# Performance work log

Hardware: AMD Instinct MI355X
Metric: run time of the kernel (lower is better)

The kernel has to match this reference:

```python
import jax, jax.numpy as jnp
import numpy as np

P = 8          # patch_size
DIM = 256      # embed dim
HEADS = 8
HEAD_DIM = DIM // HEADS
CH = 3
PATCH_DIM = CH * P * P  # 192
INNER = int(4.0 * DIM)  # 1024
SCALE = HEAD_DIM ** -0.5


def sine_pos_embedding(n, c, dtype=jnp.float32):
    # standard 1D sinusoidal position encoding, shape (n, c)
    pos = jnp.arange(n, dtype=jnp.float32)[:, None]            # (n,1)
    div = jnp.exp(jnp.arange(0, c, 2, dtype=jnp.float32) * (-np.log(10000.0) / c))
    pe = jnp.zeros((n, c), dtype=jnp.float32)
    pe = pe.at[:, 0::2].set(jnp.sin(pos * div))
    pe = pe.at[:, 1::2].set(jnp.cos(pos * div))
    return pe.astype(dtype)


def patchify(x):
    # (B,C,H,W) -> (B, n, p1*p2*C), matching 'b c (h p1) (w p2) -> b (h w) (p1 p2 c)'
    B, C, H, W = x.shape
    hp, wp = H // P, W // P
    x = x.reshape(B, C, hp, P, wp, P)
    x = x.transpose(0, 2, 4, 3, 5, 1)        # (B, hp, wp, p1, p2, C)
    return x.reshape(B, hp * wp, P * P * C)


def unpatchify(x, hp, wp):
    # (B, n, p1*p2*C) -> (B, C, H, W)
    B = x.shape[0]
    x = x.reshape(B, hp, wp, P, P, CH)
    x = x.transpose(0, 5, 1, 3, 2, 4)        # (B, C, hp, p1, wp, p2)
    return x.reshape(B, CH, hp * P, wp * P)


def setup_inputs() -> dict:
    key = jax.random.key(0)
    ks = jax.random.split(key, 16)
    B, H, W = 8, 256, 256
    s = 0.02
    img0 = jax.random.normal(ks[0], (B, CH, H, W), dtype=jnp.float32)
    img1 = jax.random.normal(ks[1], (B, CH, H, W), dtype=jnp.float32)
    mask = jax.random.randint(ks[2], (B, 1, H, W), 0, 2).astype(jnp.float32)
    return {
        "img0": img0,
        "img1": img1,
        "mask": mask,
        "w_patch": jax.random.normal(ks[3], (PATCH_DIM, DIM), jnp.float32) * s,
        "b_patch": jnp.zeros((DIM,), jnp.float32),
        "w_kv": jax.random.normal(ks[4], (DIM, 2 * DIM), jnp.float32) * s,
        "b_kv": jnp.zeros((2 * DIM,), jnp.float32),
        "w_qv": jax.random.normal(ks[5], (DIM, 2 * DIM), jnp.float32) * s,
        "b_qv": jnp.zeros((2 * DIM,), jnp.float32),
        "w_fc1": jax.random.normal(ks[6], (DIM, INNER), jnp.float32) * s,
        "b_fc1": jnp.zeros((INNER,), jnp.float32),
        "w_fc2": jax.random.normal(ks[7], (INNER, PATCH_DIM), jnp.float32) * s,
        "b_fc2": jnp.zeros((PATCH_DIM,), jnp.float32),
    }


def reference(img0, img1, mask, w_patch, b_patch, w_kv, b_kv, w_qv, b_qv,
              w_fc1, b_fc1, w_fc2, b_fc2):
    B, C, H, W = img0.shape
    hp, wp = H // P, W // P
    n = hp * wp

    x0 = patchify(img0) @ w_patch + b_patch   # (B, n, dim)
    x1 = patchify(img1) @ w_patch + b_patch
    pe = sine_pos_embedding(n, DIM)
    x0 = x0 + pe
    x1 = x1 + pe

    # img0 -> k, v
    kv = (x0 @ w_kv + b_kv).reshape(B, n, 2, HEADS, HEAD_DIM)
    kv = kv.transpose(2, 0, 3, 1, 4)          # (2, B, heads, n, hd)
    k, v = kv[0], kv[1]

    # img1 -> q (v1 unused in forward, matching torch code)
    qv = (x1 @ w_qv + b_qv).reshape(B, n, 2, DIM).transpose(2, 0, 1, 3)
    q = qv[0].reshape(B, n, HEADS, HEAD_DIM).transpose(0, 2, 1, 3)  # (B, heads, n, hd)

    dots = jnp.einsum('bhqd,bhkd->bhqk', q, k) * SCALE  # (B, heads, n, n)

    # mask: (B,1,H,W) -> per-patch sum -> binary -> additive bias over key dim
    msum = mask.reshape(B, 1, hp, P, wp, P).sum(axis=(3, 5)).reshape(B, 1, n)
    bias = jnp.where(msum > 0, 0.0, -100.0)[:, :, None, :]  # (B,1,1,n)

    attn = jax.nn.softmax(dots + bias, axis=-1)
    out = jnp.einsum('bhqk,bhkd->bhqd', attn, v)
    out = out.transpose(0, 2, 1, 3).reshape(B, n, DIM)

    # mlp2: Linear -> GELU(exact) -> Linear
    h = jax.nn.gelu(out @ w_fc1 + b_fc1, approximate=False)
    res = h @ w_fc2 + b_fc2                   # (B, n, patch_dim)

    return unpatchify(res, hp, wp)            # (B, C, H, W)
```

## Files before the change

kernel.cpp:

```cpp
#include <hip/hip_runtime.h>
#include <cstdint>
#include <cstddef>

typedef __bf16 bf16_t;
typedef uint32_t u32;
typedef __bf16 bf16x4 __attribute__((ext_vector_type(4)));
typedef __bf16 bf16x8 __attribute__((ext_vector_type(8)));
typedef float f32x4 __attribute__((ext_vector_type(4)));
typedef float f32x16 __attribute__((ext_vector_type(16)));

__device__ __forceinline__ void gload_lds16(const bf16_t* g, bf16_t* l) {
  __builtin_amdgcn_global_load_lds((const __attribute__((address_space(1))) void*)g,
                                   (__attribute__((address_space(3))) void*)l,
                                   16, 0, 0);
}

__device__ __forceinline__ f32x4 mfma16(bf16x8 a, bf16x8 b, f32x4 c) {
  return __builtin_amdgcn_mfma_f32_16x16x32_bf16(a, b, c, 0, 0, 0);
}
__device__ __forceinline__ f32x16 mfma32(bf16x8 a, bf16x8 b, f32x16 c) {
  return __builtin_amdgcn_mfma_f32_32x32x16_bf16(a, b, c, 0, 0, 0);
}

#define LOG2E 1.4426950408889634f

__global__ __launch_bounds__(256)
void prep_all(const float* __restrict__ img0, const float* __restrict__ img1,
              const float* __restrict__ mask,
              const float* __restrict__ wp, const float* __restrict__ wkv,
              const float* __restrict__ wqv, const float* __restrict__ wfc1,
              const float* __restrict__ wfc2,
              bf16_t* __restrict__ xp0, bf16_t* __restrict__ xp1,
              float* __restrict__ pe, float* __restrict__ bias,
              bf16_t* __restrict__ wpT, bf16_t* __restrict__ wkvT,
              bf16_t* __restrict__ wqT, bf16_t* __restrict__ wfc1T,
              bf16_t* __restrict__ wfc2T) {
  __shared__ float tl[64 * 65];
  int bid = blockIdx.x, tid = threadIdx.x;
  if (bid < 1536) {
    int imgsel = bid >= 768;
    int t = (bid - (imgsel ? 768 : 0)) * 256 + tid;
    const float* img = imgsel ? img1 : img0;
    bf16_t* xp = imgsel ? xp1 : xp0;
    int wpp = t & 31, p1 = (t >> 5) & 7, hp = (t >> 8) & 31, rest = t >> 13;
    int b = rest / 3, c = rest - b * 3;
    const float* src = img + (((size_t)(b * 3 + c) * 256 + hp * 8 + p1) * 256 + wpp * 8);
    float4 v0 = *(const float4*)src;
    float4 v1 = *(const float4*)(src + 4);
    int row = b * 1024 + hp * 32 + wpp;
    bf16_t* dst = xp + (size_t)row * 192 + p1 * 24 + c;
    dst[0]  = (bf16_t)v0.x; dst[3]  = (bf16_t)v0.y; dst[6]  = (bf16_t)v0.z; dst[9]  = (bf16_t)v0.w;
    dst[12] = (bf16_t)v1.x; dst[15] = (bf16_t)v1.y; dst[18] = (bf16_t)v1.z; dst[21] = (bf16_t)v1.w;
  } else if (bid < 2560) {
    int t = bid - 1536, c = tid;
    int i2 = c & ~1;
    float div = expf((float)i2 * (-9.210340371976184f / 256.0f));
    float arg = (float)t * div;
    pe[t * 256 + c] = (c & 1) ? cosf(arg) : sinf(arg);
  } else if (bid < 2592) {
    int g = (bid - 2560) * 256 + tid;
    int b = g >> 10, t = g & 1023, hp = t >> 5, wpp = t & 31;
    const float* mp = mask + ((size_t)b * 256 + hp * 8) * 256 + wpp * 8;
    float s = 0.f;
    #pragma unroll
    for (int p1 = 0; p1 < 8; p1++) {
      float4 a = *(const float4*)(mp + p1 * 256);
      float4 c = *(const float4*)(mp + p1 * 256 + 4);
      s += a.x + a.y + a.z + a.w + c.x + c.y + c.z + c.w;
    }
    bias[g] = (s > 0.f) ? 0.f : (-100.f * LOG2E);
  } else {
    int i = bid - 2592;
    const float* src; bf16_t* dst; int srcN, dstK, NT;
    if (i >= 172) {
      int j = i - 172;
      bf16_t* p = wfc2T + 192 * 1024 + j * 8192 + tid * 32;
      bf16x8 z;
      #pragma unroll
      for (int e = 0; e < 8; e++) z[e] = (bf16_t)0.0f;
      *(bf16x8*)(p) = z; *(bf16x8*)(p + 8) = z;
      *(bf16x8*)(p + 16) = z; *(bf16x8*)(p + 24) = z;
      return;
    }
    if (i < 12)       { src = wp;   dst = wpT;   srcN = 256;  dstK = 192;  NT = 4; }
    else if (i < 44)  { i -= 12;  src = wkv;  dst = wkvT;  srcN = 512;  dstK = 256;  NT = 8; }
    else if (i < 60)  { i -= 44;  src = wqv;  dst = wqT;   srcN = 512;  dstK = 256;  NT = 4; }
    else if (i < 124) { i -= 60;  src = wfc1; dst = wfc1T; srcN = 1024; dstK = 256;  NT = 16; }
    else              { i -= 124; src = wfc2; dst = wfc2T; srcN = 192;  dstK = 1024; NT = 3; }
    int kt = i / NT, nt = i - kt * NT;
    #pragma unroll
    for (int j = 0; j < 4; j++) {
      int r = (tid >> 4) + 16 * j, c = (tid & 15) * 4;
      float4 v = *(const float4*)(src + (size_t)(kt * 64 + r) * srcN + nt * 64 + c);
      tl[r * 65 + c] = v.x; tl[r * 65 + c + 1] = v.y;
      tl[r * 65 + c + 2] = v.z; tl[r * 65 + c + 3] = v.w;
    }
    __syncthreads();
    #pragma unroll
    for (int j = 0; j < 16; j++) {
      int flat = tid + 256 * j;
      int n_l = flat >> 6, k_l = flat & 63;
      dst[(size_t)(nt * 64 + n_l) * dstK + kt * 64 + k_l] = (bf16_t)tl[k_l * 65 + n_l];
    }
  }
}

template<int EPI, int BN>
__global__ __launch_bounds__(256)
void gemm_bt(const bf16_t* __restrict__ A_, const bf16_t* __restrict__ A2,
             const bf16_t* __restrict__ Bt_, const bf16_t* __restrict__ Bt2,
             int M, int N, int K,
             const float* __restrict__ bias_, const float* __restrict__ bias2,
             const float* __restrict__ pe,
             bf16_t* __restrict__ out_b, bf16_t* __restrict__ out_b2,
             bf16_t* __restrict__ out_b3, float* __restrict__ out_f) {
  constexpr int NF = BN / 32;
  __shared__ bf16_t alds[4 * 64 * 8];
  __shared__ bf16_t blds[4 * BN * 8];
  const int tid = threadIdx.x;
  const int lane = tid & 63, wid = tid >> 6;
  const int ln15 = lane & 15, hi = lane >> 4;
  const int brow = blockIdx.x * 64;
  int bcol = blockIdx.y * BN;
  const bf16_t* A = A_;
  const bf16_t* Bt = Bt_;
  const float* bias = bias_;
  bool qpart = false;
  if (EPI == 0 && blockIdx.z) A = A2;
  if (EPI == 5 && blockIdx.y >= 4) {
    qpart = true; A = A2; Bt = Bt2; bias = bias2; bcol -= 512;
  }
  const int wr = wid >> 1, wc = wid & 1;

  f32x4 acc[2][NF];
  #pragma unroll
  for (int m = 0; m < 2; m++)
    #pragma unroll
    for (int n = 0; n < NF; n++) acc[m][n] = (f32x4){0.f, 0.f, 0.f, 0.f};

  for (int k0 = 0; k0 < K; k0 += 32) {
    {
      int c = tid; int row = c & 63; int kb = c >> 6;
      const bf16_t* g = A + (size_t)(brow + row) * K + k0 + kb * 8;
      gload_lds16(g, &alds[(wid * 64) * 8]);
    }
    #pragma unroll
    for (int s = 0; s < BN / 64; s++) {
      int c = tid + s * 256; int row = c & (BN - 1); int kb = c / BN;
      const bf16_t* g = Bt + (size_t)(bcol + row) * K + k0 + kb * 8;
      gload_lds16(g, &blds[(wid * 64 + s * 256) * 8]);
    }
    __syncthreads();
    bf16x8 af[2], bfr[NF];
    #pragma unroll
    for (int m = 0; m < 2; m++)
      af[m] = *(const bf16x8*)&alds[(hi * 64 + wr * 32 + m * 16 + ln15) * 8];
    #pragma unroll
    for (int n = 0; n < NF; n++)
      bfr[n] = *(const bf16x8*)&blds[(hi * BN + wc * (BN / 2) + n * 16 + ln15) * 8];
    #pragma unroll
    for (int m = 0; m < 2; m++)
      #pragma unroll
      for (int n = 0; n < NF; n++)
        acc[m][n] = mfma16(af[m], bfr[n], acc[m][n]);
    __syncthreads();
  }

  #pragma unroll
  for (int m = 0; m < 2; m++) {
    #pragma unroll
    for (int n = 0; n < NF; n++) {
      #pragma unroll
      for (int r = 0; r < 4; r++) {
        int grow = brow + wr * 32 + m * 16 + hi * 4 + r;
        int gcol = bcol + wc * (BN / 2) + n * 16 + ln15;
        float v = acc[m][n][r];
        if (EPI == 0) {
          v += bias[gcol] + pe[(grow & 1023) * 256 + gcol];
          bf16_t* outx = blockIdx.z ? out_b2 : out_b;
          outx[(size_t)grow * N + gcol] = (bf16_t)v;
        } else if (EPI == 5) {
          v += bias[gcol];
          int b = grow >> 10, t = grow & 1023;
          if (!qpart) {
            if (gcol < 256) {
              int h = gcol >> 5, d = gcol & 31;
              out_b[(((size_t)(b * 8 + h) * 1024 + t) << 5) + d] = (bf16_t)v;
            } else {
              int c2 = gcol - 256; int h = c2 >> 5, d = c2 & 31;
              out_b2[(((size_t)(b * 8 + h) * 32 + d) << 10) + t] = (bf16_t)v;
            }
          } else {
            v *= (0.17677669529663687f * LOG2E);
            int h = gcol >> 5, d = gcol & 31;
            out_b3[(((size_t)(b * 8 + h) * 1024 + t) << 5) + d] = (bf16_t)v;
          }
        } else if (EPI == 3) {
          v += bias[gcol];
          float gg = 0.5f * v * (1.0f + erff(v * 0.7071067811865476f));
          out_b[(size_t)grow * N + gcol] = (bf16_t)gg;
        } else if (EPI == 4) {
          if (gcol < 192) {
            v += bias[gcol];
            int b = grow >> 10, t = grow & 1023;
            int hp = t >> 5, wpp = t & 31;
            int p = gcol / 3; int c = gcol - p * 3;
            int p1 = p >> 3, p2 = p & 7;
            out_f[(((size_t)(b * 3 + c) * 256 + hp * 8 + p1) * 256) + wpp * 8 + p2] = v;
          }
        }
      }
    }
  }
}

union PW { u32 w[4]; bf16x8 v; };

__device__ __forceinline__ u32 pkbf(float a, float b) {
  union { bf16_t h[2]; u32 w; } u;
  u.h[0] = (bf16_t)a; u.h[1] = (bf16_t)b;
  return u.w;
}

__device__ __forceinline__ void pl32swap(u32& a, u32& b) {
  asm volatile("v_permlane32_swap_b32 %0, %1" : "+v"(a), "+v"(b));
}

__global__ __launch_bounds__(256, 4)
void attn_kernel(const bf16_t* __restrict__ q, const bf16_t* __restrict__ k,
                 const bf16_t* __restrict__ vt, const float* __restrict__ bias,
                 bf16_t* __restrict__ out) {
  __shared__ float OL[4][32][34];
  __shared__ float LS[4][64];
  int tid = threadIdx.x, lane = tid & 63, wid = tid >> 6;
  int l31 = lane & 31, g = lane >> 5;
  int x = blockIdx.x & 7;
  int bh = (((blockIdx.x >> 3) & 7) << 3) | x;
  int qt = blockIdx.x >> 6;
  int b = bh >> 3, h = bh & 7;
  int q0 = qt * 32;
  const bf16_t* qp = q + ((size_t)bh * 1024 + q0 + l31) * 32;
  bf16x8 qf0 = *(const bf16x8*)(qp + g * 8);
  bf16x8 qf1 = *(const bf16x8*)(qp + 16 + g * 8);
  const bf16_t* kbase = k + (size_t)bh * 32768;
  const bf16_t* vbase = vt + (size_t)bh * 32768;
  const float* bb = bias + b * 1024;

  f32x16 acc;
  #pragma unroll
  for (int r = 0; r < 16; r++) acc[r] = 0.f;
  float lsum = 0.f;

  #pragma unroll
  for (int kt = 0; kt < 8; kt++) {
    int k0 = (wid * 8 + kt) * 32;
    bf16x8 kA = *(const bf16x8*)(kbase + (size_t)(k0 + l31) * 32 + g * 8);
    bf16x8 kB = *(const bf16x8*)(kbase + (size_t)(k0 + l31) * 32 + 16 + g * 8);
    bf16x8 vA = *(const bf16x8*)(vbase + (size_t)l31 * 1024 + k0 + g * 8);
    bf16x8 vB = *(const bf16x8*)(vbase + (size_t)l31 * 1024 + k0 + 16 + g * 8);
    f32x4 c0 = *(const f32x4*)(bb + k0 + 4 * g);
    f32x4 c1 = *(const f32x4*)(bb + k0 + 8 + 4 * g);
    f32x4 c2 = *(const f32x4*)(bb + k0 + 16 + 4 * g);
    f32x4 c3 = *(const f32x4*)(bb + k0 + 24 + 4 * g);
    f32x16 S;
    S[0] = c0[0]; S[1] = c0[1]; S[2] = c0[2]; S[3] = c0[3];
    S[4] = c1[0]; S[5] = c1[1]; S[6] = c1[2]; S[7] = c1[3];
    S[8] = c2[0]; S[9] = c2[1]; S[10] = c2[2]; S[11] = c2[3];
    S[12] = c3[0]; S[13] = c3[1]; S[14] = c3[2]; S[15] = c3[3];
    S = mfma32(kA, qf0, S);
    S = mfma32(kB, qf1, S);
    float p[16];
    #pragma unroll
    for (int r = 0; r < 16; r++) p[r] = exp2f(S[r]);
    lsum += (((p[0] + p[1]) + (p[2] + p[3])) + ((p[4] + p[5]) + (p[6] + p[7]))) +
            (((p[8] + p[9]) + (p[10] + p[11])) + ((p[12] + p[13]) + (p[14] + p[15])));
    u32 w[8];
    #pragma unroll
    for (int j = 0; j < 8; j++) w[j] = pkbf(p[2 * j], p[2 * j + 1]);
    u32 xa = w[2], ya = w[0]; pl32swap(xa, ya);
    u32 xb = w[3], yb = w[1]; pl32swap(xb, yb);
    u32 xc = w[6], yc = w[4]; pl32swap(xc, yc);
    u32 xd = w[7], yd = w[5]; pl32swap(xd, yd);
    PW A0, A1;
    A0.w[0] = g ? xa : w[0];  A0.w[2] = g ? w[2] : ya;
    A0.w[1] = g ? xb : w[1];  A0.w[3] = g ? w[3] : yb;
    A1.w[0] = g ? xc : w[4];  A1.w[2] = g ? w[6] : yc;
    A1.w[1] = g ? xd : w[5];  A1.w[3] = g ? w[7] : yd;
    acc = mfma32(A0.v, vA, acc);
    acc = mfma32(A1.v, vB, acc);
  }

  #pragma unroll
  for (int r = 0; r < 16; r++) {
    int row = (r & 3) + 8 * (r >> 2) + 4 * g;
    OL[wid][row][l31] = acc[r];
  }
  LS[wid][lane] = lsum;
  __syncthreads();

  int qq = tid >> 3, d0 = (tid & 7) * 4;
  float l = 0.f;
  #pragma unroll
  for (int w2 = 0; w2 < 4; w2++) l += LS[w2][qq] + LS[w2][32 + qq];
  float o0 = 0.f, o1 = 0.f, o2 = 0.f, o3 = 0.f;
  #pragma unroll
  for (int w2 = 0; w2 < 4; w2++) {
    o0 += OL[w2][qq][d0];     o1 += OL[w2][qq][d0 + 1];
    o2 += OL[w2][qq][d0 + 2]; o3 += OL[w2][qq][d0 + 3];
  }
  float linv = 1.f / l;
  bf16x4 ov;
  ov[0] = (bf16_t)(o0 * linv); ov[1] = (bf16_t)(o1 * linv);
  ov[2] = (bf16_t)(o2 * linv); ov[3] = (bf16_t)(o3 * linv);
  *(bf16x4*)(out + ((size_t)b * 1024 + q0 + qq) * 256 + h * 32 + d0) = ov;
}

extern "C" void kernel_launch(void* const* d_in, const int* in_sizes, int n_in,
                              void* d_out, int out_size, void* d_ws, size_t ws_size,
                              hipStream_t stream) {
  (void)in_sizes; (void)n_in; (void)out_size; (void)ws_size;
  const float* img0    = (const float*)d_in[0];
  const float* img1    = (const float*)d_in[1];
  const float* mask    = (const float*)d_in[2];
  const float* w_patch = (const float*)d_in[3];
  const float* b_patch = (const float*)d_in[4];
  const float* w_kv    = (const float*)d_in[5];
  const float* b_kv    = (const float*)d_in[6];
  const float* w_qv    = (const float*)d_in[7];
  const float* b_qv    = (const float*)d_in[8];
  const float* w_fc1   = (const float*)d_in[9];
  const float* b_fc1   = (const float*)d_in[10];
  const float* w_fc2   = (const float*)d_in[11];
  const float* b_fc2   = (const float*)d_in[12];
  float* out = (float*)d_out;

  char* ws = (char*)d_ws;
  float*  pe    = (float*)(ws + 0);
  float*  bias  = (float*)(ws + 1048576);
  bf16_t* wpT   = (bf16_t*)(ws + 1081344);
  bf16_t* wkvT  = (bf16_t*)(ws + 1179648);
  bf16_t* wqT   = (bf16_t*)(ws + 1441792);
  bf16_t* wfc1T = (bf16_t*)(ws + 1572864);
  bf16_t* wfc2T = (bf16_t*)(ws + 2097152);
  bf16_t* xp0   = (bf16_t*)(ws + 2621440);
  bf16_t* xp1   = (bf16_t*)(ws + 5767168);
  bf16_t* x0    = (bf16_t*)(ws + 8912896);
  bf16_t* x1    = (bf16_t*)(ws + 13107200);
  bf16_t* kbuf  = (bf16_t*)(ws + 17301504);
  bf16_t* vtbuf = (bf16_t*)(ws + 21495808);
  bf16_t* qbuf  = (bf16_t*)(ws + 25690112);
  bf16_t* aout  = (bf16_t*)(ws + 29884416);
  bf16_t* hbuf  = (bf16_t*)(ws + 34078720);

  prep_all<<<2772, 256, 0, stream>>>(img0, img1, mask, w_patch, w_kv, w_qv, w_fc1, w_fc2,
                                     xp0, xp1, pe, bias, wpT, wkvT, wqT, wfc1T, wfc2T);

  gemm_bt<0, 64><<<dim3(128, 4, 2), 256, 0, stream>>>(xp0, xp1, wpT, nullptr, 8192, 256, 192,
                                                      b_patch, nullptr, pe, x0, x1, nullptr, nullptr);
  gemm_bt<5, 128><<<dim3(128, 6), 256, 0, stream>>>(x0, x1, wkvT, wqT, 8192, 512, 256,
                                                    b_kv, b_qv, nullptr, kbuf, vtbuf, qbuf, nullptr);

  attn_kernel<<<2048, 256, 0, stream>>>(qbuf, kbuf, vtbuf, bias, aout);

  gemm_bt<3, 128><<<dim3(128, 8), 256, 0, stream>>>(aout, nullptr, wfc1T, nullptr, 8192, 1024, 256,
                                                    b_fc1, nullptr, nullptr, hbuf, nullptr, nullptr, nullptr);
  gemm_bt<4, 64><<<dim3(128, 4), 256, 0, stream>>>(hbuf, nullptr, wfc2T, nullptr, 8192, 256, 1024,
                                                   b_fc2, nullptr, nullptr, nullptr, nullptr, nullptr, out);
}
```

Baseline: 122.9 us.

## Stage K/V tiles in LDS with double buffering and share them across query waves

The attention kernel is restructured. Before, each block of four waves split the 1024 keys for 32 queries and combined partial outputs through shared memory. Now each block covers 128 queries, one 32-query tile per wave, and every wave walks all keys. K and V^T chunks of 256 keys are staged into double-buffered, XOR-swizzled LDS with global_load_lds, so all four waves reuse the same K/V data. This removes the cross-wave output reduction and cuts global K/V traffic, but it uses more LDS, lowers occupancy to two blocks per CU, and launches four times fewer blocks.

```diff
diff --git a/kernel.cpp b/kernel.cpp
--- a/kernel.cpp
+++ b/kernel.cpp
@@ -226,19 +226,39 @@
   asm volatile("v_permlane32_swap_b32 %0, %1" : "+v"(a), "+v"(b));
 }
 
-__global__ __launch_bounds__(256, 4)
+__device__ __forceinline__ void stage_kv(const bf16_t* kbase, const bf16_t* vbase,
+                                         int ch, bf16_t* kl, bf16_t* vl,
+                                         int tid, int wid) {
+  #pragma unroll
+  for (int p = 0; p < 4; p++) {
+    int s = p * 256 + tid;
+    int row = s >> 2, cs = (s & 3) ^ (row & 3);
+    const bf16_t* src = kbase + (size_t)(ch * 256 + row) * 32 + cs * 8;
+    gload_lds16(src, kl + (size_t)(p * 256 + wid * 64) * 8);
+  }
+  #pragma unroll
+  for (int p = 0; p < 4; p++) {
+    int s = p * 256 + tid;
+    int row = s >> 5, cs = (s & 31) ^ row;
+    const bf16_t* src = vbase + (size_t)row * 1024 + ch * 256 + cs * 8;
+    gload_lds16(src, vl + (size_t)(p * 256 + wid * 64) * 8);
+  }
+}
+
+__global__ __launch_bounds__(256, 2)
 void attn_kernel(const bf16_t* __restrict__ q, const bf16_t* __restrict__ k,
                  const bf16_t* __restrict__ vt, const float* __restrict__ bias,
                  bf16_t* __restrict__ out) {
-  __shared__ float OL[4][32][34];
-  __shared__ float LS[4][64];
+  __shared__ bf16_t klds[2][1024 * 8];
+  __shared__ bf16_t vlds[2][1024 * 8];
+  __shared__ float LSL[4][32];
   int tid = threadIdx.x, lane = tid & 63, wid = tid >> 6;
   int l31 = lane & 31, g = lane >> 5;
-  int x = blockIdx.x & 7;
-  int bh = (((blockIdx.x >> 3) & 7) << 3) | x;
-  int qt = blockIdx.x >> 6;
+  int x = blockIdx.x & 7, idx = blockIdx.x >> 3;
+  int qt = idx & 7;
+  int bh = ((idx >> 3) << 3) | x;
   int b = bh >> 3, h = bh & 7;
-  int q0 = qt * 32;
+  int q0 = qt * 128 + wid * 32;
   const bf16_t* qp = q + ((size_t)bh * 1024 + q0 + l31) * 32;
   bf16x8 qf0 = *(const bf16x8*)(qp + g * 8);
   bf16x8 qf1 = *(const bf16x8*)(qp + 16 + g * 8);
@@ -251,68 +271,65 @@
   for (int r = 0; r < 16; r++) acc[r] = 0.f;
   float lsum = 0.f;
 
-  #pragma unroll
-  for (int kt = 0; kt < 8; kt++) {
-    int k0 = (wid * 8 + kt) * 32;
-    bf16x8 kA = *(const bf16x8*)(kbase + (size_t)(k0 + l31) * 32 + g * 8);
-    bf16x8 kB = *(const bf16x8*)(kbase + (size_t)(k0 + l31) * 32 + 16 + g * 8);
-    bf16x8 vA = *(const bf16x8*)(vbase + (size_t)l31 * 1024 + k0 + g * 8);
-    bf16x8 vB = *(const bf16x8*)(vbase + (size_t)l31 * 1024 + k0 + 16 + g * 8);
-    f32x4 c0 = *(const f32x4*)(bb + k0 + 4 * g);
-    f32x4 c1 = *(const f32x4*)(bb + k0 + 8 + 4 * g);
-    f32x4 c2 = *(const f32x4*)(bb + k0 + 16 + 4 * g);
-    f32x4 c3 = *(const f32x4*)(bb + k0 + 24 + 4 * g);
-    f32x16 S;
-    S[0] = c0[0]; S[1] = c0[1]; S[2] = c0[2]; S[3] = c0[3];
-    S[4] = c1[0]; S[5] = c1[1]; S[6] = c1[2]; S[7] = c1[3];
-    S[8] = c2[0]; S[9] = c2[1]; S[10] = c2[2]; S[11] = c2[3];
-    S[12] = c3[0]; S[13] = c3[1]; S[14] = c3[2]; S[15] = c3[3];
-    S = mfma32(kA, qf0, S);
-    S = mfma32(kB, qf1, S);
-    float p[16];
-    #pragma unroll
-    for (int r = 0; r < 16; r++) p[r] = exp2f(S[r]);
-    lsum += (((p[0] + p[1]) + (p[2] + p[3])) + ((p[4] + p[5]) + (p[6] + p[7]))) +
-            (((p[8] + p[9]) + (p[10] + p[11])) + ((p[12] + p[13]) + (p[14] + p[15])));
-    u32 w[8];
-    #pragma unroll
-    for (int j = 0; j < 8; j++) w[j] = pkbf(p[2 * j], p[2 * j + 1]);
-    u32 xa = w[2], ya = w[0]; pl32swap(xa, ya);
-    u32 xb = w[3], yb = w[1]; pl32swap(xb, yb);
-    u32 xc = w[6], yc = w[4]; pl32swap(xc, yc);
-    u32 xd = w[7], yd = w[5]; pl32swap(xd, yd);
-    PW A0, A1;
-    A0.w[0] = g ? xa : w[0];  A0.w[2] = g ? w[2] : ya;
-    A0.w[1] = g ? xb : w[1];  A0.w[3] = g ? w[3] : yb;
-    A1.w[0] = g ? xc : w[4];  A1.w[2] = g ? w[6] : yc;
-    A1.w[1] = g ? xd : w[5];  A1.w[3] = g ? w[7] : yd;
-    acc = mfma32(A0.v, vA, acc);
-    acc = mfma32(A1.v, vB, acc);
-  }
-
+  stage_kv(kbase, vbase, 0, klds[0], vlds[0], tid, wid);
+  __syncthreads();
+
+  int cur = 0;
+  for (int ch = 0; ch < 4; ch++) {
+    if (ch < 3) stage_kv(kbase, vbase, ch + 1, klds[cur ^ 1], vlds[cur ^ 1], tid, wid);
+    const bf16_t* kl = klds[cur];
+    const bf16_t* vl = vlds[cur];
+    #pragma unroll
+    for (int kt = 0; kt < 8; kt++) {
+      int row0 = kt * 32 + l31;
+      bf16x8 kA = *(const bf16x8*)(kl + (size_t)(row0 * 4 + (g ^ (row0 & 3))) * 8);
+      bf16x8 kB = *(const bf16x8*)(kl + (size_t)(row0 * 4 + ((2 + g) ^ (row0 & 3))) * 8);
+      bf16x8 vA = *(const bf16x8*)(vl + (size_t)(l31 * 32 + ((4 * kt + g) ^ l31)) * 8);
+      bf16x8 vB = *(const bf16x8*)(vl + (size_t)(l31 * 32 + ((4 * kt + 2 + g) ^ l31)) * 8);
+      int K0 = ch * 256 + kt * 32;
+      f32x4 c0 = *(const f32x4*)(bb + K0 + 4 * g);
+      f32x4 c1 = *(const f32x4*)(bb + K0 + 8 + 4 * g);
+      f32x4 c2 = *(const f32x4*)(bb + K0 + 16 + 4 * g);
+      f32x4 c3 = *(const f32x4*)(bb + K0 + 24 + 4 * g);
+      f32x16 S;
+      S[0] = c0[0]; S[1] = c0[1]; S[2] = c0[2]; S[3] = c0[3];
+      S[4] = c1[0]; S[5] = c1[1]; S[6] = c1[2]; S[7] = c1[3];
+      S[8] = c2[0]; S[9] = c2[1]; S[10] = c2[2]; S[11] = c2[3];
+      S[12] = c3[0]; S[13] = c3[1]; S[14] = c3[2]; S[15] = c3[3];
+      S = mfma32(kA, qf0, S);
+      S = mfma32(kB, qf1, S);
+      float p[16];
+      #pragma unroll
+      for (int r = 0; r < 16; r++) p[r] = exp2f(S[r]);
+      lsum += (((p[0] + p[1]) + (p[2] + p[3])) + ((p[4] + p[5]) + (p[6] + p[7]))) +
+              (((p[8] + p[9]) + (p[10] + p[11])) + ((p[12] + p[13]) + (p[14] + p[15])));
+      u32 w[8];
+      #pragma unroll
+      for (int j = 0; j < 8; j++) w[j] = pkbf(p[2 * j], p[2 * j + 1]);
+      u32 xa = w[2], ya = w[0]; pl32swap(xa, ya);
+      u32 xb = w[3], yb = w[1]; pl32swap(xb, yb);
+      u32 xc = w[6], yc = w[4]; pl32swap(xc, yc);
+      u32 xd = w[7], yd = w[5]; pl32swap(xd, yd);
+      PW A0, A1;
+      A0.w[0] = g ? xa : w[0];  A0.w[2] = g ? w[2] : ya;
+      A0.w[1] = g ? xb : w[1];  A0.w[3] = g ? w[3] : yb;
+      A1.w[0] = g ? xc : w[4];  A1.w[2] = g ? w[6] : yc;
+      A1.w[1] = g ? xd : w[5];  A1.w[3] = g ? w[7] : yd;
+      acc = mfma32(A0.v, vA, acc);
+      acc = mfma32(A1.v, vB, acc);
+    }
+    __syncthreads();
+    cur ^= 1;
+  }
+
+  lsum += __shfl_xor(lsum, 32);
+  LSL[wid][l31] = lsum;
   #pragma unroll
   for (int r = 0; r < 16; r++) {
     int row = (r & 3) + 8 * (r >> 2) + 4 * g;
-    OL[wid][row][l31] = acc[r];
-  }
-  LS[wid][lane] = lsum;
-  __syncthreads();
-
-  int qq = tid >> 3, d0 = (tid & 7) * 4;
-  float l = 0.f;
-  #pragma unroll
-  for (int w2 = 0; w2 < 4; w2++) l += LS[w2][qq] + LS[w2][32 + qq];
-  float o0 = 0.f, o1 = 0.f, o2 = 0.f, o3 = 0.f;
-  #pragma unroll
-  for (int w2 = 0; w2 < 4; w2++) {
-    o0 += OL[w2][qq][d0];     o1 += OL[w2][qq][d0 + 1];
-    o2 += OL[w2][qq][d0 + 2]; o3 += OL[w2][qq][d0 + 3];
-  }
-  float linv = 1.f / l;
-  bf16x4 ov;
-  ov[0] = (bf16_t)(o0 * linv); ov[1] = (bf16_t)(o1 * linv);
-  ov[2] = (bf16_t)(o2 * linv); ov[3] = (bf16_t)(o3 * linv);
-  *(bf16x4*)(out + ((size_t)b * 1024 + q0 + qq) * 256 + h * 32 + d0) = ov;
+    float linv = 1.f / LSL[wid][row];
+    out[((size_t)b * 1024 + q0 + row) * 256 + h * 32 + l31] = (bf16_t)(acc[r] * linv);
+  }
 }
 
 extern "C" void kernel_launch(void* const* d_in, const int* in_sizes, int n_in,
@@ -360,7 +377,7 @@
   gemm_bt<5, 128><<<dim3(128, 6), 256, 0, stream>>>(x0, x1, wkvT, wqT, 8192, 512, 256,
                                                     b_kv, b_qv, nullptr, kbuf, vtbuf, qbuf, nullptr);
 
-  attn_kernel<<<2048, 256, 0, stream>>>(qbuf, kbuf, vtbuf, bias, aout);
+  attn_kernel<<<512, 256, 0, stream>>>(qbuf, kbuf, vtbuf, bias, aout);
 
   gemm_bt<3, 128><<<dim3(128, 8), 256, 0, stream>>>(aout, nullptr, wfc1T, nullptr, 8192, 1024, 256,
                                                     b_fc1, nullptr, nullptr, hbuf, nullptr, nullptr, nullptr);
```

Result: no change. 121.9 us (-0.8%).
